# Kernel tuning notes

Measured on AMD Instinct MI355X. Metric: run time of the kernel, lower is better.

## Reference

```python
import jax, jax.numpy as jnp
import numpy as np

B, T, F = 512, 1024, 8
H1, H2 = 70, 21   # '80k' config, bidirectional
D1, D2 = 30, 20


def _u(key, shape, fan):
    s = 1.0 / np.sqrt(fan)
    return jax.random.uniform(key, shape, jnp.float32, -s, s)


def setup_inputs() -> dict:
    key = jax.random.key(0)
    ks = iter(jax.random.split(key, 32))
    inp = {"x": jax.random.normal(next(ks), (B, T, F), jnp.float32)}
    # LSTM layer 1 (input F -> H1), forward and backward directions; torch gate order i,f,g,o
    for d in ("f", "b"):
        inp[f"w_ih1_{d}"] = _u(next(ks), (4 * H1, F), H1)
        inp[f"w_hh1_{d}"] = _u(next(ks), (4 * H1, H1), H1)
        inp[f"b_ih1_{d}"] = _u(next(ks), (4 * H1,), H1)
        inp[f"b_hh1_{d}"] = _u(next(ks), (4 * H1,), H1)
    # LSTM layer 2 (input 2*H1 -> H2)
    for d in ("f", "b"):
        inp[f"w_ih2_{d}"] = _u(next(ks), (4 * H2, 2 * H1), H2)
        inp[f"w_hh2_{d}"] = _u(next(ks), (4 * H2, H2), H2)
        inp[f"b_ih2_{d}"] = _u(next(ks), (4 * H2,), H2)
        inp[f"b_hh2_{d}"] = _u(next(ks), (4 * H2,), H2)
    # Dense head: 2*H2 -> D1 -> D2 -> 1
    inp["d1_w"] = _u(next(ks), (D1, 2 * H2), 2 * H2)
    inp["d1_b"] = _u(next(ks), (D1,), 2 * H2)
    inp["d2_w"] = _u(next(ks), (D2, D1), D1)
    inp["d2_b"] = _u(next(ks), (D2,), D1)
    inp["out_w"] = _u(next(ks), (1, D2), D2)
    inp["out_b"] = _u(next(ks), (1,), D2)
    return inp


def _lstm_dir(x, w_ih, w_hh, b_ih, b_hh, reverse):
    # x: [B, T, Fin]; torch LSTM gate order: i, f, g, o
    if reverse:
        x = x[:, ::-1]
    H = w_hh.shape[1]
    pre = jnp.einsum('btf,gf->btg', x, w_ih) + b_ih + b_hh  # [B, T, 4H]
    pre_t = jnp.moveaxis(pre, 1, 0)                          # [T, B, 4H]

    def step(carry, p):
        h, c = carry
        g = p + h @ w_hh.T
        i, f, gg, o = jnp.split(g, 4, axis=-1)
        c = jax.nn.sigmoid(f) * c + jax.nn.sigmoid(i) * jnp.tanh(gg)
        h = jax.nn.sigmoid(o) * jnp.tanh(c)
        return (h, c), h

    init = (jnp.zeros((x.shape[0], H), x.dtype), jnp.zeros((x.shape[0], H), x.dtype))
    _, hs = jax.lax.scan(step, init, pre_t)
    hs = jnp.moveaxis(hs, 0, 1)  # [B, T, H]
    if reverse:
        hs = hs[:, ::-1]
    return hs


def _bilstm(x, wf, uf, bif, bhf, wb, ub, bib, bhb):
    return jnp.concatenate([
        _lstm_dir(x, wf, uf, bif, bhf, reverse=False),
        _lstm_dir(x, wb, ub, bib, bhb, reverse=True),
    ], axis=-1)


def reference(x,
              w_ih1_f, w_hh1_f, b_ih1_f, b_hh1_f,
              w_ih1_b, w_hh1_b, b_ih1_b, b_hh1_b,
              w_ih2_f, w_hh2_f, b_ih2_f, b_hh2_f,
              w_ih2_b, w_hh2_b, b_ih2_b, b_hh2_b,
              d1_w, d1_b, d2_w, d2_b, out_w, out_b):
    h = _bilstm(x, w_ih1_f, w_hh1_f, b_ih1_f, b_hh1_f,
                w_ih1_b, w_hh1_b, b_ih1_b, b_hh1_b)   # [B, T, 2*H1]
    h = _bilstm(h, w_ih2_f, w_hh2_f, b_ih2_f, b_hh2_f,
                w_ih2_b, w_hh2_b, b_ih2_b, b_hh2_b)   # [B, T, 2*H2]
    h = jax.nn.relu(h @ d1_w.T + d1_b)
    h = jax.nn.relu(h @ d2_w.T + d2_b)
    return h @ out_w.T + out_b                          # [B, T, 1]
```

## Files before the change

### kernel.cpp

```cpp
#include <hip/hip_runtime.h>


typedef _Float16 v2f16 __attribute__((ext_vector_type(2)));
typedef _Float16 v4h   __attribute__((ext_vector_type(4)));
typedef _Float16 v8h   __attribute__((ext_vector_type(8)));
typedef float    f32x4 __attribute__((ext_vector_type(4)));

__device__ __forceinline__ float fdot2(v2f16 a, v2f16 b, float c) {
  return __builtin_amdgcn_fdot2(a, b, c, false);
}
#if __has_builtin(__builtin_amdgcn_rcpf)
__device__ __forceinline__ float rcpf(float x) { return __builtin_amdgcn_rcpf(x); }
#else
__device__ __forceinline__ float rcpf(float x) { return 1.f / x; }
#endif

__device__ __forceinline__ void lds_barrier() {
  asm volatile("s_waitcnt lgkmcnt(0)" ::: "memory");
  __builtin_amdgcn_s_barrier();
  __builtin_amdgcn_sched_barrier(0);
}

#define O_W1M  0u
#define O_WP2  110592u
#define O_W2M  118656u
#define O_BIAS 177792u
#define O_DATA 178496u

__global__ void pack_kernel(const float* __restrict__ wihf, const float* __restrict__ whhf,
                            const float* __restrict__ wihb, const float* __restrict__ whhb,
                            const float* __restrict__ b1if, const float* __restrict__ b1hf,
                            const float* __restrict__ b1ib, const float* __restrict__ b1hb,
                            const float* __restrict__ wih2f, const float* __restrict__ wih2b,
                            const float* __restrict__ whh2f, const float* __restrict__ whh2b,
                            const float* __restrict__ bif, const float* __restrict__ bhf,
                            const float* __restrict__ bib, const float* __restrict__ bhb,
                            char* __restrict__ ws) {
  _Float16* w1m = (_Float16*)(ws + O_W1M);
  _Float16* wp2 = (_Float16*)(ws + O_WP2);
  _Float16* w2m = (_Float16*)(ws + O_W2M);
  float* biasc = (float*)(ws + O_BIAS);
  int idx = blockIdx.x * 256 + threadIdx.x;
  if (idx < 55296) {
    int d = idx / 27648, rem = idx % 27648, rp = rem / 96, k = rem % 96;
    int u = rp >> 2, g = rp & 3;
    const float* wih = d ? wihb : wihf;
    const float* whh = d ? whhb : whhf;
    const float* bi = d ? b1ib : b1if;
    const float* bh = d ? b1hb : b1hf;
    float v = 0.f;
    if (u < 70) {
      int src = g * 70 + u;
      if (k < 8) v = wih[src * 8 + k];
      else if (k < 78) v = whh[src * 70 + (k - 8)];
      else if (k == 78) v = bi[src] + bh[src];
    }
    w1m[idx] = (_Float16)v;
  } else if (idx < 59328) {
    int j = idx - 55296;
    int d = j / 2016, rem = j % 2016, r = rem / 24, k = rem % 24;
    const float* whh = d ? whh2b : whh2f;
    wp2[j] = (_Float16)((k < 21) ? whh[r * 21 + k] : 0.f);
  } else if (idx < 88896) {
    int j = idx - 59328;
    int n = j / 168, k = j % 168;
    float v = 0.f;
    if (k < 140) {
      if (n < 84) v = wih2f[n * 140 + k];
      else if (n < 168) v = wih2b[(n - 84) * 140 + k];
    }
    w2m[j] = (_Float16)v;
  } else if (idx < 89072) {
    int n = idx - 88896;
    float v = 0.f;
    if (n < 84) v = bif[n] + bhf[n];
    else if (n < 168) v = bib[n - 84] + bhb[n - 84];
    biasc[n] = v;
  }
}

__global__ __launch_bounds__(384) void lstm1_kernel(
    const float* __restrict__ x,
    const _Float16* __restrict__ w1m,
    _Float16* __restrict__ h1, int b0, int nb) {
  __shared__ __align__(16) _Float16 km[2][16][104];
  const int tid = threadIdx.x;
  const int wv = tid >> 6, lane = tid & 63;
  const int q = lane >> 4, bc = lane & 15;
  const int d = blockIdx.y;
  const int blg = blockIdx.x * 16;
  const int gb0 = b0 + blg;

  for (int i = tid; i < 2 * 16 * 104; i += 384) ((_Float16*)km)[i] = (_Float16)0.f;

  if (d == 0) {
    for (int i = tid; i < 16 * 1024 * 5; i += 384) {
      int t = i / 80, r = i - t * 80;
      int b = r / 5, j = r - b * 5;
      v4h z = {(_Float16)0.f, (_Float16)0.f, (_Float16)0.f, (_Float16)0.f};
      *(v4h*)&h1[((size_t)t * nb + blg + b) * 176 + 140 + j * 4] = z;
    }
  }

  v8h af[3][3];
#pragma unroll
  for (int i = 0; i < 3; ++i) {
    int T = wv + 6 * i;
#pragma unroll
    for (int kc = 0; kc < 3; ++kc)
      af[i][kc] = *(const v8h*)&w1m[(size_t)(d * 288 + T * 16 + bc) * 96 + kc * 32 + q * 8];
  }
  const int U0 = wv * 4 + q;

  __syncthreads();

  if (tid < 16) {
    km[0][tid][78] = (_Float16)1.f;
    km[1][tid][78] = (_Float16)1.f;
  }
  if (tid < 32) {
    int b = tid >> 1, half = tid & 1;
    int t0 = d ? 1023 : 0;
    float4 xv = *(const float4*)&x[((size_t)(gb0 + b) * 1024 + t0) * 8 + half * 4];
    v4h xh; xh[0] = (_Float16)xv.x; xh[1] = (_Float16)xv.y;
    xh[2] = (_Float16)xv.z; xh[3] = (_Float16)xv.w;
    *(v4h*)&km[0][b][half * 4] = xh;
  }
  float c0 = 0.f, c1 = 0.f, c2 = 0.f;
  __syncthreads();

#pragma unroll 1
  for (int s = 0; s < 1024; ++s) {
    const int cur = s & 1, nxt = cur ^ 1;
    float4 xv;
    const bool xl = (tid < 32) && (s < 1023);
    if (xl) {
      int tn = d ? (1022 - s) : (s + 1);
      xv = *(const float4*)&x[((size_t)(gb0 + (tid >> 1)) * 1024 + tn) * 8 + (tid & 1) * 4];
    }
    v8h bf0 = *(const v8h*)&km[cur][bc][q * 8];
    v8h bf1 = *(const v8h*)&km[cur][bc][32 + q * 8];
    v8h bf2 = *(const v8h*)&km[cur][bc][64 + q * 8];
    f32x4 z4 = (f32x4){0.f, 0.f, 0.f, 0.f};
    f32x4 A0 = __builtin_amdgcn_mfma_f32_16x16x32_f16(af[0][0], bf0, z4, 0, 0, 0);
    f32x4 A1 = __builtin_amdgcn_mfma_f32_16x16x32_f16(af[1][0], bf0, z4, 0, 0, 0);
    f32x4 A2 = __builtin_amdgcn_mfma_f32_16x16x32_f16(af[2][0], bf0, z4, 0, 0, 0);
    A0 = __builtin_amdgcn_mfma_f32_16x16x32_f16(af[0][1], bf1, A0, 0, 0, 0);
    A1 = __builtin_amdgcn_mfma_f32_16x16x32_f16(af[1][1], bf1, A1, 0, 0, 0);
    A2 = __builtin_amdgcn_mfma_f32_16x16x32_f16(af[2][1], bf1, A2, 0, 0, 0);
    A0 = __builtin_amdgcn_mfma_f32_16x16x32_f16(af[0][2], bf2, A0, 0, 0, 0);
    A1 = __builtin_amdgcn_mfma_f32_16x16x32_f16(af[1][2], bf2, A1, 0, 0, 0);
    A2 = __builtin_amdgcn_mfma_f32_16x16x32_f16(af[2][2], bf2, A2, 0, 0, 0);
    const int te = d ? (1023 - s) : s;
    const size_t rowb = ((size_t)te * nb + blg + bc) * 176 + d * 70;

#define GATE(Ai, ci, ioff)                                                   \
    {                                                                        \
      float ai = rcpf(1.f + __expf(-Ai[0]));                                 \
      float afv = rcpf(1.f + __expf(-Ai[1]));                                \
      float ag = fmaf(2.f, rcpf(1.f + __expf(-2.f * Ai[2])), -1.f);          \
      float ao = rcpf(1.f + __expf(-Ai[3]));                                 \
      ci = fmaf(afv, ci, ai * ag);                                           \
      float hv = ao * fmaf(2.f, rcpf(1.f + __expf(-2.f * ci)), -1.f);        \
      int U = U0 + ioff;                                                     \
      if (U < 70) {                                                          \
        _Float16 hh = (_Float16)hv;                                          \
        km[nxt][bc][8 + U] = hh;                                             \
        h1[rowb + U] = hh;                                                   \
      }                                                                      \
    }
    GATE(A0, c0, 0)
    GATE(A1, c1, 24)
    GATE(A2, c2, 48)
#undef GATE
    if (xl) {
      v4h xh; xh[0] = (_Float16)xv.x; xh[1] = (_Float16)xv.y;
      xh[2] = (_Float16)xv.z; xh[3] = (_Float16)xv.w;
      *(v4h*)&km[nxt][tid >> 1][(tid & 1) * 4] = xh;
    }
    lds_barrier();
  }
}

__global__ __launch_bounds__(256) void pre2_kernel(
    _Float16* __restrict__ h1, const char* __restrict__ ws) {
  const _Float16* w2m = (const _Float16*)(ws + O_W2M);
  const float* biasc = (const float*)(ws + O_BIAS);
  __shared__ _Float16 Al[64][184];
  __shared__ float Bl[176];
  const int tid = threadIdx.x;
  const int r0 = blockIdx.x * 64;
#pragma unroll
  for (int i = 0; i < 6; ++i) {
    int cid = i * 256 + tid;
    if (cid < 1408) {
      int row = cid / 22, ch = cid % 22;
      *(v8h*)&Al[row][ch * 8] = *(const v8h*)&h1[(size_t)(r0 + row) * 176 + ch * 8];
    }
  }
  if (tid < 176) Bl[tid] = biasc[tid];
  __syncthreads();

  const int wv = tid >> 6, lane = tid & 63;
  const int ml = lane & 15, kq = lane >> 4;
  v8h af[5];
#pragma unroll
  for (int k = 0; k < 5; ++k)
    af[k] = *(const v8h*)&Al[wv * 16 + ml][k * 32 + kq * 8];

  const v8h* wg = (const v8h*)w2m;
  f32x4 acc[11];
#pragma unroll
  for (int ct = 0; ct < 11; ++ct) acc[ct] = (f32x4){0.f, 0.f, 0.f, 0.f};

  v8h bc[5], bn[5];
#pragma unroll
  for (int k = 0; k < 5; ++k) bn[k] = wg[(size_t)ml * 21 + k * 4 + kq];
#pragma unroll
  for (int ct = 0; ct < 11; ++ct) {
#pragma unroll
    for (int k = 0; k < 5; ++k) bc[k] = bn[k];
    if (ct < 10) {
#pragma unroll
      for (int k = 0; k < 5; ++k) bn[k] = wg[(size_t)((ct + 1) * 16 + ml) * 21 + k * 4 + kq];
    }
#pragma unroll
    for (int k = 0; k < 5; ++k)
      acc[ct] = __builtin_amdgcn_mfma_f32_16x16x32_f16(af[k], bc[k], acc[ct], 0, 0, 0);
  }
  __syncthreads();
#pragma unroll
  for (int ct = 0; ct < 11; ++ct) {
#pragma unroll
    for (int r = 0; r < 4; ++r) {
      int row = wv * 16 + kq * 4 + r, col = ct * 16 + ml;
      Al[row][col] = (_Float16)(acc[ct][r] + Bl[col]);
    }
  }
  __syncthreads();
#pragma unroll
  for (int i = 0; i < 6; ++i) {
    int cid = i * 256 + tid;
    if (cid < 1408) {
      int row = cid / 22, ch = cid % 22;
      *(v8h*)&h1[(size_t)(r0 + row) * 176 + ch * 8] = *(const v8h*)&Al[row][ch * 8];
    }
  }
}

__global__ __launch_bounds__(64) void lstm2_kernel(
    const _Float16* __restrict__ pre2, const _Float16* __restrict__ wp2,
    _Float16* __restrict__ h2, int nb) {
  __shared__ __align__(16) _Float16 kv[2][32];
  const int lane = threadIdx.x;
  const int bl = blockIdx.x;
  const int d = blockIdx.y;
  const int u = lane >> 1, p = lane & 1;
  const bool active = lane < 42;

  ((_Float16*)kv)[lane] = (_Float16)0.f;

  v2f16 w0[12], w1[12];
  if (active) {
    const v8h* wr0 = (const v8h*)&wp2[(d * 84 + (2 * p) * 21 + u) * 24];
    const v8h* wr1 = (const v8h*)&wp2[(d * 84 + (2 * p + 1) * 21 + u) * 24];
#pragma unroll
    for (int ch = 0; ch < 3; ++ch) {
      v8h a = wr0[ch], b = wr1[ch];
#pragma unroll
      for (int q = 0; q < 4; ++q) {
        v2f16 t0; t0[0] = a[2 * q]; t0[1] = a[2 * q + 1]; w0[ch * 4 + q] = t0;
        v2f16 t1; t1[0] = b[2 * q]; t1[1] = b[2 * q + 1]; w1[ch * 4 + q] = t1;
      }
    }
  }
  const int col0 = d * 84 + (2 * p) * 21 + u;
  const int col1 = col0 + 21;
  const ptrdiff_t dlt = (ptrdiff_t)(d ? -nb : nb) * 176;
  const _Float16* pp = pre2 + ((size_t)(d ? 1023 : 0) * (size_t)nb + bl) * 176;

  _Float16 pa0 = pp[col0],            pa1 = pp[col1];
  _Float16 pb0 = (pp + dlt)[col0],    pb1 = (pp + dlt)[col1];
  _Float16 pc0 = (pp + 2*dlt)[col0],  pc1 = (pp + 2*dlt)[col1];
  _Float16 pd0 = (pp + 3*dlt)[col0],  pd1 = (pp + 3*dlt)[col1];
  const _Float16* pf = pp + 4 * dlt;

  const float esc0 = p ? -2.f : -1.f;
  const float ym0  = p ?  2.f :  1.f;
  const float ya0  = p ? -1.f :  0.f;
  float cc = 0.f;
  int s = 0;

#define L2STEP(P0, P1)                                                      \
  {                                                                         \
    const int cur = s & 1, nxt = cur ^ 1;                                   \
    float A0v = (float)P0, A1v = (float)P1;                                 \
    const float4* kp = (const float4*)&kv[cur][0];                          \
    float4 q0 = kp[0], q1 = kp[1], q2 = kp[2];                              \
    float x0 = A0v, x1 = 0.f, x2 = 0.f, x3 = 0.f;                           \
    float z0 = A1v, z1 = 0.f, z2 = 0.f, z3 = 0.f;                           \
    x0 = fdot2(__builtin_bit_cast(v2f16, q0.x), w0[0], x0);                 \
    x1 = fdot2(__builtin_bit_cast(v2f16, q0.y), w0[1], x1);                 \
    x2 = fdot2(__builtin_bit_cast(v2f16, q0.z), w0[2], x2);                 \
    x3 = fdot2(__builtin_bit_cast(v2f16, q0.w), w0[3], x3);                 \
    x0 = fdot2(__builtin_bit_cast(v2f16, q1.x), w0[4], x0);                 \
    x1 = fdot2(__builtin_bit_cast(v2f16, q1.y), w0[5], x1);                 \
    x2 = fdot2(__builtin_bit_cast(v2f16, q1.z), w0[6], x2);                 \
    x3 = fdot2(__builtin_bit_cast(v2f16, q1.w), w0[7], x3);                 \
    x0 = fdot2(__builtin_bit_cast(v2f16, q2.x), w0[8], x0);                 \
    x1 = fdot2(__builtin_bit_cast(v2f16, q2.y), w0[9], x1);                 \
    x2 = fdot2(__builtin_bit_cast(v2f16, q2.z), w0[10], x2);                \
    x3 = fdot2(__builtin_bit_cast(v2f16, q2.w), w0[11], x3);                \
    z0 = fdot2(__builtin_bit_cast(v2f16, q0.x), w1[0], z0);                 \
    z1 = fdot2(__builtin_bit_cast(v2f16, q0.y), w1[1], z1);                 \
    z2 = fdot2(__builtin_bit_cast(v2f16, q0.z), w1[2], z2);                 \
    z3 = fdot2(__builtin_bit_cast(v2f16, q0.w), w1[3], z3);                 \
    z0 = fdot2(__builtin_bit_cast(v2f16, q1.x), w1[4], z0);                 \
    z1 = fdot2(__builtin_bit_cast(v2f16, q1.y), w1[5], z1);                 \
    z2 = fdot2(__builtin_bit_cast(v2f16, q1.z), w1[6], z2);                 \
    z3 = fdot2(__builtin_bit_cast(v2f16, q1.w), w1[7], z3);                 \
    z0 = fdot2(__builtin_bit_cast(v2f16, q2.x), w1[8], z0);                 \
    z1 = fdot2(__builtin_bit_cast(v2f16, q2.y), w1[9], z1);                 \
    z2 = fdot2(__builtin_bit_cast(v2f16, q2.z), w1[10], z2);                \
    z3 = fdot2(__builtin_bit_cast(v2f16, q2.w), w1[11], z3);                \
    float A = (x0 + x1) + (x2 + x3), Bv = (z0 + z1) + (z2 + z3);            \
    float Y0 = fmaf(ym0, rcpf(1.f + __expf(A * esc0)), ya0);                \
    float Y1 = rcpf(1.f + __expf(-Bv));                                     \
    float Zs = __shfl_xor(Y0, 1);                                           \
    float Ws = __shfl_xor(Y1, 1);                                           \
    float ai = p ? Zs : Y0;                                                 \
    float af = p ? Ws : Y1;                                                 \
    float ag = p ? Y0 : Zs;                                                 \
    float ao = p ? Y1 : Ws;                                                 \
    cc = fmaf(af, cc, ai * ag);                                             \
    float tc = fmaf(2.f, rcpf(1.f + __expf(-2.f * cc)), -1.f);              \
    float hv = ao * tc;                                                     \
    if (active && p == 0) {                                                 \
      _Float16 hh = (_Float16)hv;                                           \
      int te = d ? (1023 - s) : s;                                          \
      kv[nxt][u] = hh;                                                      \
      h2[((size_t)te * nb + bl) * 48 + d * 21 + u] = hh;                    \
    }                                                                       \
    if (s < 1020) { P0 = pf[col0]; P1 = pf[col1]; }                         \
    pf += dlt;                                                              \
    ++s;                                                                    \
  }

#pragma unroll 1
  for (int it = 0; it < 256; ++it) {
    L2STEP(pa0, pa1)
    L2STEP(pb0, pb1)
    L2STEP(pc0, pc1)
    L2STEP(pd0, pd1)
  }
#undef L2STEP
}

__global__ __launch_bounds__(256) void head_kernel(
    const _Float16* __restrict__ h2,
    const float* __restrict__ d1w, const float* __restrict__ d1b,
    const float* __restrict__ d2w, const float* __restrict__ d2b,
    const float* __restrict__ ow, const float* __restrict__ ob,
    float* __restrict__ out, int b0, int lognb) {
  int n = blockIdx.x * 256 + threadIdx.x;
  int t = n >> lognb, bl = n & ((1 << lognb) - 1);
  const v8h* hp = (const v8h*)&h2[(size_t)n * 48];
  float in[48];
#pragma unroll
  for (int i = 0; i < 6; ++i) {
    v8h hc = hp[i];
#pragma unroll
    for (int j = 0; j < 8; ++j) in[i * 8 + j] = (float)hc[j];
  }
  float a1[30];
#pragma unroll
  for (int cc = 0; cc < 30; ++cc) {
    float a = d1b[cc];
#pragma unroll
    for (int k = 0; k < 42; ++k) a += in[k] * d1w[cc * 42 + k];
    a1[cc] = fmaxf(a, 0.f);
  }
  float a2[20];
#pragma unroll
  for (int cc = 0; cc < 20; ++cc) {
    float a = d2b[cc];
#pragma unroll
    for (int k = 0; k < 30; ++k) a += a1[k] * d2w[cc * 30 + k];
    a2[cc] = fmaxf(a, 0.f);
  }
  float o = ob[0];
#pragma unroll
  for (int k = 0; k < 20; ++k) o += a2[k] * ow[k];
  out[(size_t)(b0 + bl) * 1024 + t] = o;
}

extern "C" void kernel_launch(void* const* d_in, const int* in_sizes, int n_in,
                              void* d_out, int out_size, void* d_ws, size_t ws_size,
                              hipStream_t stream) {
  const float* x = (const float*)d_in[0];
  const float* wih1f = (const float*)d_in[1];
  const float* whh1f = (const float*)d_in[2];
  const float* bih1f = (const float*)d_in[3];
  const float* bhh1f = (const float*)d_in[4];
  const float* wih1b = (const float*)d_in[5];
  const float* whh1b = (const float*)d_in[6];
  const float* bih1b = (const float*)d_in[7];
  const float* bhh1b = (const float*)d_in[8];
  const float* wih2f = (const float*)d_in[9];
  const float* whh2f = (const float*)d_in[10];
  const float* bih2f = (const float*)d_in[11];
  const float* bhh2f = (const float*)d_in[12];
  const float* wih2b = (const float*)d_in[13];
  const float* whh2b = (const float*)d_in[14];
  const float* bih2b = (const float*)d_in[15];
  const float* bhh2b = (const float*)d_in[16];
  const float* d1w = (const float*)d_in[17];
  const float* d1b = (const float*)d_in[18];
  const float* d2w = (const float*)d_in[19];
  const float* d2b = (const float*)d_in[20];
  const float* ow = (const float*)d_in[21];
  const float* ob = (const float*)d_in[22];
  float* out = (float*)d_out;
  char* wsb = (char*)d_ws;

  const int cands[6] = {1, 2, 4, 8, 16, 32};
  int nslice = 32;
  for (int i = 0; i < 6; ++i) {
    size_t rows = (size_t)(512 / cands[i]) * 1024;
    if (O_DATA + rows * 448 <= ws_size) { nslice = cands[i]; break; }
  }
  const int nb = 512 / nslice;
  int lognb = 0; while ((1 << lognb) < nb) ++lognb;
  const size_t rows = (size_t)nb * 1024;

  _Float16* w1m = (_Float16*)(wsb + O_W1M);
  _Float16* wp2 = (_Float16*)(wsb + O_WP2);
  _Float16* h1  = (_Float16*)(wsb + O_DATA);
  _Float16* h2  = (_Float16*)(wsb + O_DATA + rows * 352);

  pack_kernel<<<348, 256, 0, stream>>>(wih1f, whh1f, wih1b, whh1b,
                                       bih1f, bhh1f, bih1b, bhh1b,
                                       wih2f, wih2b, whh2f, whh2b,
                                       bih2f, bhh2f, bih2b, bhh2b, wsb);

  for (int s = 0; s < nslice; ++s) {
    const int b0 = s * nb;
    lstm1_kernel<<<dim3(nb / 16, 2), 384, 0, stream>>>(x, w1m, h1, b0, nb);
    pre2_kernel<<<nb * 16, 256, 0, stream>>>(h1, wsb);
    lstm2_kernel<<<dim3(nb, 2), 64, 0, stream>>>(h1, wp2, h2, nb);
    head_kernel<<<nb * 4, 256, 0, stream>>>(h2, d1w, d1b, d2w, d2b, ow, ob,
                                            out, b0, lognb);
  }
}
```

Measured before the change: 1.445 ms.

## Spread layer-1 LSTM gate tiles over 12 waves and fold exp scaling into weights

Layer-1 LSTM blocks grow from 6 to 12 wavefronts, so each wave handles one or two gate tiles instead of three. This shortens the serial per-step MFMA and activation chain, at the cost of more barrier participants. The log2(e) factors are pre-multiplied into the packed weights and bias so the gate nonlinearities can use raw exp2. The zero-fill of h1 padding columns is removed, and pre2 instead masks the padded K columns in its last A fragment.

```diff
diff --git a/kernel.cpp b/kernel.cpp
--- a/kernel.cpp
+++ b/kernel.cpp
@@ -14,6 +14,13 @@
 #else
 __device__ __forceinline__ float rcpf(float x) { return 1.f / x; }
 #endif
+__device__ __forceinline__ float ex2(float v) {
+#if __has_builtin(__builtin_amdgcn_exp2f)
+  return __builtin_amdgcn_exp2f(v);
+#else
+  return __expf(v * 0.6931471805599453f);
+#endif
+}
 
 __device__ __forceinline__ void lds_barrier() {
   asm volatile("s_waitcnt lgkmcnt(0)" ::: "memory");
@@ -51,9 +58,10 @@
     float v = 0.f;
     if (u < 70) {
       int src = g * 70 + u;
-      if (k < 8) v = wih[src * 8 + k];
-      else if (k < 78) v = whh[src * 70 + (k - 8)];
-      else if (k == 78) v = bi[src] + bh[src];
+      float scale = (g == 2) ? 2.8853900817779268f : 1.4426950408889634f;
+      if (k < 8) v = wih[src * 8 + k] * scale;
+      else if (k < 78) v = whh[src * 70 + (k - 8)] * scale;
+      else if (k == 78) v = (bi[src] + bh[src]) * scale;
     }
     w1m[idx] = (_Float16)v;
   } else if (idx < 59328) {
@@ -79,38 +87,35 @@
   }
 }
 
-__global__ __launch_bounds__(384) void lstm1_kernel(
+__global__ __launch_bounds__(768) void lstm1_kernel(
     const float* __restrict__ x,
     const _Float16* __restrict__ w1m,
     _Float16* __restrict__ h1, int b0, int nb) {
   __shared__ __align__(16) _Float16 km[2][16][104];
   const int tid = threadIdx.x;
-  const int wv = tid >> 6, lane = tid & 63;
+  const int w = tid >> 6, lane = tid & 63;
   const int q = lane >> 4, bc = lane & 15;
   const int d = blockIdx.y;
   const int blg = blockIdx.x * 16;
   const int gb0 = b0 + blg;
 
-  for (int i = tid; i < 2 * 16 * 104; i += 384) ((_Float16*)km)[i] = (_Float16)0.f;
-
-  if (d == 0) {
-    for (int i = tid; i < 16 * 1024 * 5; i += 384) {
-      int t = i / 80, r = i - t * 80;
-      int b = r / 5, j = r - b * 5;
-      v4h z = {(_Float16)0.f, (_Float16)0.f, (_Float16)0.f, (_Float16)0.f};
-      *(v4h*)&h1[((size_t)t * nb + blg + b) * 176 + 140 + j * 4] = z;
-    }
-  }
-
-  v8h af[3][3];
-#pragma unroll
-  for (int i = 0; i < 3; ++i) {
-    int T = wv + 6 * i;
-#pragma unroll
-    for (int kc = 0; kc < 3; ++kc)
-      af[i][kc] = *(const v8h*)&w1m[(size_t)(d * 288 + T * 16 + bc) * 96 + kc * 32 + q * 8];
-  }
-  const int U0 = wv * 4 + q;
+  for (int i = tid; i < 2 * 16 * 104; i += 768) ((_Float16*)km)[i] = (_Float16)0.f;
+
+  int nt, T0;
+  if (w < 4)       { nt = 1; T0 = w; }
+  else if (w < 10) { nt = 2; T0 = 4 + 2 * (w - 4); }
+  else             { nt = 1; T0 = 16 + (w - 10); }
+
+  v8h af[2][3];
+#pragma unroll
+  for (int i = 0; i < 2; ++i) {
+    if (i < nt) {
+      int T = T0 + i;
+#pragma unroll
+      for (int kc = 0; kc < 3; ++kc)
+        af[i][kc] = *(const v8h*)&w1m[(size_t)(d * 288 + T * 16 + bc) * 96 + kc * 32 + q * 8];
+    }
+  }
 
   __syncthreads();
 
@@ -126,7 +131,7 @@
     xh[2] = (_Float16)xv.z; xh[3] = (_Float16)xv.w;
     *(v4h*)&km[0][b][half * 4] = xh;
   }
-  float c0 = 0.f, c1 = 0.f, c2 = 0.f;
+  float c0 = 0.f, c1 = 0.f;
   __syncthreads();
 
 #pragma unroll 1
@@ -143,35 +148,36 @@
     v8h bf2 = *(const v8h*)&km[cur][bc][64 + q * 8];
     f32x4 z4 = (f32x4){0.f, 0.f, 0.f, 0.f};
     f32x4 A0 = __builtin_amdgcn_mfma_f32_16x16x32_f16(af[0][0], bf0, z4, 0, 0, 0);
-    f32x4 A1 = __builtin_amdgcn_mfma_f32_16x16x32_f16(af[1][0], bf0, z4, 0, 0, 0);
-    f32x4 A2 = __builtin_amdgcn_mfma_f32_16x16x32_f16(af[2][0], bf0, z4, 0, 0, 0);
+    f32x4 A1 = z4;
+    if (nt == 2) A1 = __builtin_amdgcn_mfma_f32_16x16x32_f16(af[1][0], bf0, z4, 0, 0, 0);
     A0 = __builtin_amdgcn_mfma_f32_16x16x32_f16(af[0][1], bf1, A0, 0, 0, 0);
-    A1 = __builtin_amdgcn_mfma_f32_16x16x32_f16(af[1][1], bf1, A1, 0, 0, 0);
-    A2 = __builtin_amdgcn_mfma_f32_16x16x32_f16(af[2][1], bf1, A2, 0, 0, 0);
+    if (nt == 2) A1 = __builtin_amdgcn_mfma_f32_16x16x32_f16(af[1][1], bf1, A1, 0, 0, 0);
     A0 = __builtin_amdgcn_mfma_f32_16x16x32_f16(af[0][2], bf2, A0, 0, 0, 0);
-    A1 = __builtin_amdgcn_mfma_f32_16x16x32_f16(af[1][2], bf2, A1, 0, 0, 0);
-    A2 = __builtin_amdgcn_mfma_f32_16x16x32_f16(af[2][2], bf2, A2, 0, 0, 0);
+    if (nt == 2) A1 = __builtin_amdgcn_mfma_f32_16x16x32_f16(af[1][2], bf2, A1, 0, 0, 0);
     const int te = d ? (1023 - s) : s;
     const size_t rowb = ((size_t)te * nb + blg + bc) * 176 + d * 70;
 
-#define GATE(Ai, ci, ioff)                                                   \
+#define GATE(Ai, ci, U)                                                      \
     {                                                                        \
-      float ai = rcpf(1.f + __expf(-Ai[0]));                                 \
-      float afv = rcpf(1.f + __expf(-Ai[1]));                                \
-      float ag = fmaf(2.f, rcpf(1.f + __expf(-2.f * Ai[2])), -1.f);          \
-      float ao = rcpf(1.f + __expf(-Ai[3]));                                 \
-      ci = fmaf(afv, ci, ai * ag);                                           \
-      float hv = ao * fmaf(2.f, rcpf(1.f + __expf(-2.f * ci)), -1.f);        \
-      int U = U0 + ioff;                                                     \
-      if (U < 70) {                                                          \
+      float ei = ex2(-Ai[0]);                                                \
+      float ef = ex2(-Ai[1]);                                                \
+      float eg = ex2(-Ai[2]);                                                \
+      float eo = ex2(-Ai[3]);                                                \
+      float si = rcpf(1.f + ei);                                             \
+      float sf = rcpf(1.f + ef);                                             \
+      float tg = fmaf(2.f, rcpf(1.f + eg), -1.f);                            \
+      float so = rcpf(1.f + eo);                                             \
+      ci = fmaf(sf, ci, si * tg);                                            \
+      float ec = ex2(ci * -2.8853900817779268f);                             \
+      float hv = so * fmaf(2.f, rcpf(1.f + ec), -1.f);                       \
+      if ((U) < 70) {                                                        \
         _Float16 hh = (_Float16)hv;                                          \
-        km[nxt][bc][8 + U] = hh;                                             \
-        h1[rowb + U] = hh;                                                   \
+        km[nxt][bc][8 + (U)] = hh;                                           \
+        h1[rowb + (U)] = hh;                                                 \
       }                                                                      \
     }
-    GATE(A0, c0, 0)
-    GATE(A1, c1, 24)
-    GATE(A2, c2, 48)
+    GATE(A0, c0, T0 * 4 + q)
+    if (nt == 2) GATE(A1, c1, (T0 + 1) * 4 + q)
 #undef GATE
     if (xl) {
       v4h xh; xh[0] = (_Float16)xv.x; xh[1] = (_Float16)xv.y;
@@ -205,8 +211,19 @@
   const int ml = lane & 15, kq = lane >> 4;
   v8h af[5];
 #pragma unroll
-  for (int k = 0; k < 5; ++k)
+  for (int k = 0; k < 4; ++k)
     af[k] = *(const v8h*)&Al[wv * 16 + ml][k * 32 + kq * 8];
+  {
+    v8h a4 = *(const v8h*)&Al[wv * 16 + ml][128 + kq * 8];
+    if (kq >= 2) {
+#pragma unroll
+      for (int j = 0; j < 8; ++j) a4[j] = (_Float16)0.f;
+    } else if (kq == 1) {
+#pragma unroll
+      for (int j = 4; j < 8; ++j) a4[j] = (_Float16)0.f;
+    }
+    af[4] = a4;
+  }
 
   const v8h* wg = (const v8h*)w2m;
   f32x4 acc[11];
@@ -445,7 +462,7 @@
 
   for (int s = 0; s < nslice; ++s) {
     const int b0 = s * nb;
-    lstm1_kernel<<<dim3(nb / 16, 2), 384, 0, stream>>>(x, w1m, h1, b0, nb);
+    lstm1_kernel<<<dim3(nb / 16, 2), 768, 0, stream>>>(x, w1m, h1, b0, nb);
     pre2_kernel<<<nb * 16, 256, 0, stream>>>(h1, wsb);
     lstm2_kernel<<<dim3(nb, 2), 64, 0, stream>>>(h1, wp2, h2, nb);
     head_kernel<<<nb * 4, 256, 0, stream>>>(h2, d1w, d1b, d2w, d2b, ow, ob,
```

Measured after the change: 1.383 ms. 4.3% less time.
